# Kernel tuning notes

Measured on AMD Instinct MI355X. Metric: run time of the kernel, lower is better.

## Reference

```python
import jax, jax.numpy as jnp
import numpy as np

K = 3          # kernel_size (forced by hardcoded padding=1 in query unfold)
PAD = 1        # padding
C_IN = 64      # conv in_channels (x has C_IN + 5 channels)
C_OUT = 128    # out_channels
B, H, W = 16, 32, 32


def unfold(x, k, pad=0, mode='constant'):
    """torch.nn.functional.unfold equivalent. x: (B,C,H,W) -> (B, C*k*k, L).
    Ordering matches torch: channel slowest, then kernel row, then kernel col."""
    if pad:
        x = jnp.pad(x, ((0, 0), (0, 0), (pad, pad), (pad, pad)), mode=mode)
    b, c, h, w = x.shape
    oh, ow = h - k + 1, w - k + 1
    # (B, C, k*k, oh, ow) with patch index i*k+j
    patches = jnp.stack([x[:, :, i:i + oh, j:j + ow]
                         for i in range(k) for j in range(k)], axis=2)
    return patches.reshape(b, c * k * k, oh * ow)


def conv2d(x, w, b, pad):
    out = jax.lax.conv_general_dilated(
        x, w, window_strides=(1, 1), padding=[(pad, pad), (pad, pad)],
        dimension_numbers=('NCHW', 'OIHW', 'NCHW'))
    return out + b[None, :, None, None]


def setup_inputs() -> dict:
    key = jax.random.key(0)
    ks = jax.random.split(key, 6)
    fan1 = C_IN * K * K
    fan2 = C_OUT * 1 * 1
    return {
        'x': jax.random.normal(ks[0], (B, C_IN + 5, H, W), jnp.float32),
        'conv_w': jax.random.normal(ks[1], (C_OUT, C_IN, K, K), jnp.float32) / np.sqrt(fan1),
        'conv_b': jax.random.normal(ks[2], (C_OUT,), jnp.float32) * 0.01,
        'conv2_w': jax.random.normal(ks[3], (1, C_OUT, 1, 1), jnp.float32) / np.sqrt(fan2),
        'conv2_b': jax.random.normal(ks[4], (1,), jnp.float32) * 0.01,
        'shapes_kernel': jax.random.uniform(ks[5], (1, C_OUT, K * K * 5, 1), jnp.float32),
    }


def reference(x, conv_w, conv_b, conv2_w, conv2_b, shapes_kernel):
    k, pad = K, PAD
    center = k * k // 2

    conv_out = conv2d(x[:, :-5], conv_w, conv_b, pad)          # (B, C_OUT, H', W')
    b, cout, oh, ow = conv_out.shape
    L = oh * ow

    # shape-channel windows (replication-padded), center-relative positions
    sw = unfold(x[:, -5:], k, pad, 'edge').reshape(b, 5, k * k, L)
    sw = sw.at[:, 0:2].add(-sw[:, 0:2, center:center + 1])

    # L1 distance of each window to each learned shape kernel
    sd = jnp.abs(sw.reshape(b, 1, 5 * k * k, L) - shapes_kernel).sum(axis=2)  # (B, C_OUT, L)
    sd = sd.reshape(b, cout, oh, ow)

    saf = jax.nn.relu(conv_out / (sd + 1.0))                    # shape_attended_features

    q = conv2d(saf, conv2_w, conv2_b, 0) / jnp.sqrt(jnp.float32(cout))  # (B, 1, H', W')
    qu = jax.nn.softmax(unfold(q, k, 1), axis=1)[:, None]       # (B, 1, k*k, L), zero-padded

    u_mean = unfold(x[:, -5:-3], k, pad, 'edge').reshape(b, 2, k * k, L)
    means = (u_mean * qu).sum(axis=2)                           # (B, 2, L)

    v1 = (unfold(x[:, -3:-1], k, pad, 'edge').reshape(b, 2, k * k, L) * qu).sum(axis=2)
    v2 = (((u_mean - means[:, :, None, :]) ** 2) * qu).sum(axis=2)
    var = v1 + v2                                               # (B, 2, L)

    c1 = (unfold(x[:, -1:], k, pad, 'edge').reshape(b, 1, k * k, L) * qu).sum(axis=2)
    c2 = ((u_mean[:, 0:1] - means[:, 0:1, None, :]) *
          (u_mean[:, 1:2] - means[:, 1:2, None, :]) * qu).sum(axis=2)
    covar = c1 + c2                                             # (B, 1, L)

    agg = jnp.concatenate([means, var, covar], axis=1).reshape(b, 5, oh, ow)
    return jnp.concatenate([saf, agg], axis=1)                  # (B, C_OUT+5, H', W')
```

## Files before the change

kernel.cpp:

```cpp
#include <hip/hip_runtime.h>
#include <math.h>

#define CI 64
#define CO 128
#define CX 69
#define LPIX 1024

typedef __attribute__((ext_vector_type(8))) short bf16x8;
typedef __attribute__((ext_vector_type(4))) float f32x4;

#define WMF_OFF  0
#define SKT_OFF  147456
#define QP_OFF   (147456 + 23040)

__device__ __forceinline__ unsigned short f2bf(float f) {
  unsigned u = __float_as_uint(f);
  unsigned r = (u + 0x7fffu + ((u >> 16) & 1u)) >> 16;
  return (unsigned short)r;
}

__launch_bounds__(256)
__global__ void prepW(const float* __restrict__ cwg,
                      const float* __restrict__ skg,
                      unsigned short* __restrict__ wmf,
                      float* __restrict__ skt) {
  int i = blockIdx.x * 256 + threadIdx.x;
  if (i < 9 * 128 * 64) {
    int tap = i >> 13;
    int rem = i & 8191;
    int co = rem >> 6, cis = rem & 63;
    int ci = cis ^ ((co & 7) << 3);
    wmf[i] = f2bf(cwg[co * 576 + ci * 9 + tap]);
  } else {
    int d = i - 9 * 128 * 64;
    if (d < 45 * 128) {
      int j = d >> 7, co = d & 127;
      skt[j * 128 + co] = skg[co * 45 + j];
    }
  }
}

__launch_bounds__(256, 3)
__global__ void convFused(const float* __restrict__ xg,
                          const unsigned short* __restrict__ wmf,
                          const float* __restrict__ cbg,
                          const float* __restrict__ w2g,
                          const float* __restrict__ sktg,
                          float* __restrict__ qp,
                          float* __restrict__ outg) {
  __shared__ char arena[16384];
  __shared__ unsigned short ldsB[4 * 36 * 64];
  __shared__ float lds_sx[5 * 144];
  __shared__ float qred[4][64];

  unsigned short* A0 = (unsigned short*)arena;
  float* lds_c = (float*)arena;

  const int tid = threadIdx.x;
  const int blk = blockIdx.x;
  const int coh = blk & 1;
  const int rp  = (blk >> 1) & 15;
  const int b   = blk >> 5;
  const int r0  = rp * 2;

  const int w    = tid >> 6;
  const int lane = tid & 63;
  const int rsel = w >> 1;
  const int cq   = w & 1;
  const int n16  = lane & 15;
  const int kq   = lane >> 4;

  const float* xb = xg + (size_t)b * CX * LPIX;
  const float* xs = xb + CI * LPIX;

  {
    const int col = tid & 31;
    const int grp = tid >> 5;
    const int slot = col + 1;
    const int swk = (slot & 7) << 3;
    #pragma unroll
    for (int it = 0; it < 16; ++it) {
      const int rc  = grp + it * 8;
      const int row = rc >> 5;
      const int ci  = (rc & 31) * 2;
      const int grow = r0 - 1 + row;
      unsigned v = 0;
      if ((unsigned)grow < 32u) {
        float f0 = xb[ci * LPIX + grow * 32 + col];
        float f1 = xb[(ci + 1) * LPIX + grow * 32 + col];
        v = (unsigned)f2bf(f0) | ((unsigned)f2bf(f1) << 16);
      }
      const int gslot = ((ci >> 3) << 3) ^ swk;
      ((unsigned*)ldsB)[(((row * 36 + slot) << 6) + gslot + (ci & 7)) >> 1] = v;
    }
    for (int idx = tid; idx < 512; idx += 256) {
      const int row = idx >> 7;
      const int s4  = (idx >> 5) & 3;
      const int sl  = (s4 == 0) ? 0 : (32 + s4);
      const int ci  = (idx & 31) * 2;
      const int gsl = ((ci >> 3) << 3) ^ ((sl & 7) << 3);
      ((unsigned*)ldsB)[(((row * 36 + sl) << 6) + gsl + (ci & 7)) >> 1] = 0;
    }
  }

  for (int idx = tid; idx < 5 * 144; idx += 256) {
    int c = idx / 144, rem = idx - c * 144;
    int s = rem / 36, j = rem - s * 36;
    int hh = r0 - 1 + s; hh = hh < 0 ? 0 : (hh > 31 ? 31 : hh);
    int col = j - 1;     col = col < 0 ? 0 : (col > 31 ? 31 : col);
    lds_sx[idx] = xs[c * LPIX + hh * 32 + col];
  }

  {
    const uint4* s = (const uint4*)(wmf + (size_t)(coh * 64) * 64);
    uint4 v0 = s[tid], v1 = s[tid + 256];
    uint4* d = (uint4*)A0;
    d[tid] = v0; d[tid + 256] = v1;
  }
  __syncthreads();

  f32x4 acc[2][2] = {};

  for (int tap = 0; tap < 9; ++tap) {
    const int dr = tap / 3, dc = tap % 3;
    uint4 pf0, pf1;
    if (tap < 8) {
      const uint4* s = (const uint4*)(wmf + (size_t)((tap + 1) * 128 + coh * 64) * 64);
      pf0 = s[tid]; pf1 = s[tid + 256];
    }
    const int rowst = rsel + dr;
    const unsigned short* abase = A0 + (tap & 1) * 4096;
    #pragma unroll
    for (int ci0 = 0; ci0 < 64; ci0 += 32) {
      const int g = (ci0 >> 3) + kq;
      bf16x8 bfr[2];
      #pragma unroll
      for (int t = 0; t < 2; ++t) {
        const int slot = t * 16 + n16 + dc;
        const int gs = (g ^ (slot & 7)) << 3;
        bfr[t] = *(const bf16x8*)(ldsB + ((rowst * 36 + slot) << 6) + gs);
      }
      const int gsa = ((kq | (ci0 >> 3)) ^ (n16 & 7)) << 3;
      #pragma unroll
      for (int ct = 0; ct < 2; ++ct) {
        const int co_l = cq * 32 + ct * 16 + n16;
        bf16x8 a = *(const bf16x8*)(abase + co_l * 64 + gsa);
        acc[0][ct] = __builtin_amdgcn_mfma_f32_16x16x32_bf16(a, bfr[0], acc[0][ct], 0, 0, 0);
        acc[1][ct] = __builtin_amdgcn_mfma_f32_16x16x32_bf16(a, bfr[1], acc[1][ct], 0, 0, 0);
      }
    }
    if (tap < 8) {
      uint4* d = (uint4*)(A0 + ((tap + 1) & 1) * 4096);
      d[tid] = pf0; d[tid + 256] = pf1;
    }
    __syncthreads();
  }

  #pragma unroll
  for (int pt = 0; pt < 2; ++pt) {
    const int pxl = rsel * 32 + pt * 16 + n16;
    #pragma unroll
    for (int ct = 0; ct < 2; ++ct) {
      const int cog = cq * 8 + ct * 4 + kq;
      const int sg  = cog ^ (pxl & 7);
      *(f32x4*)&lds_c[pxl * 64 + sg * 4] = acc[pt][ct];
    }
  }
  __syncthreads();

  const int wS   = __builtin_amdgcn_readfirstlane(w);
  const int co0g = coh * 64 + wS * 16;
  const int pxl  = lane;

  float cvals[16];
  #pragma unroll
  for (int g = 0; g < 4; ++g) {
    const int cog = wS * 4 + g;
    const int sg  = cog ^ (pxl & 7);
    *(f32x4*)&cvals[g * 4] = *(const f32x4*)&lds_c[pxl * 64 + sg * 4];
  }

  const int xbase = (pxl >> 5) * 36 + (pxl & 31);
  float swv[45];
  {
    const float c0 = lds_sx[0 * 144 + 37 + xbase];
    const float c1 = lds_sx[1 * 144 + 37 + xbase];
    #pragma unroll
    for (int c = 0; c < 5; ++c) {
      float ctr = (c == 0) ? c0 : ((c == 1) ? c1 : 0.f);
      #pragma unroll
      for (int s = 0; s < 3; ++s)
        #pragma unroll
        for (int dc = 0; dc < 3; ++dc)
          swv[c * 9 + s * 3 + dc] = lds_sx[c * 144 + s * 36 + dc + xbase] - ctr;
    }
  }

  float sd[16];
  #pragma unroll
  for (int k = 0; k < 16; ++k) sd[k] = 0.f;
  const float* skt = sktg + co0g;
  #pragma unroll
  for (int j = 0; j < 45; ++j) {
    const float sv = swv[j];
    #pragma unroll
    for (int k = 0; k < 16; ++k)
      sd[k] += fabsf(sv - skt[j * 128 + k]);
  }

  float qpv = 0.f;
  float* ob = outg + ((size_t)b * 133 + co0g) * LPIX + (r0 + (pxl >> 5)) * 32 + (pxl & 31);
  #pragma unroll
  for (int k = 0; k < 16; ++k) {
    float v = (cvals[k] + cbg[co0g + k]) * __builtin_amdgcn_rcpf(sd[k] + 1.0f);
    v = v > 0.f ? v : 0.f;
    ob[(size_t)k * LPIX] = v;
    qpv = fmaf(v, w2g[co0g + k], qpv);
  }

  qred[w][lane] = qpv;
  __syncthreads();
  if (tid < 64) {
    float q = qred[0][tid] + qred[1][tid] + qred[2][tid] + qred[3][tid];
    qp[coh * 16384 + b * LPIX + r0 * 32 + tid] = q;
  }
}

__launch_bounds__(64)
__global__ void statsB(const float* __restrict__ xg,
                       const float* __restrict__ qp,
                       const float* __restrict__ b2g,
                       float* __restrict__ outg) {
  const int gid = blockIdx.x * 64 + threadIdx.x;
  const int b = gid >> 10;
  const int h = (gid >> 5) & 31;
  const int w = gid & 31;

  const float b2 = b2g[0];
  const float* q0 = qp + (size_t)b * LPIX;
  float qv[9];
  float m = -1e30f;
  #pragma unroll
  for (int t = 0; t < 9; ++t) {
    int hh = h + t / 3 - 1, wc = w + t % 3 - 1;
    float v = 0.f;
    if ((unsigned)hh < 32u && (unsigned)wc < 32u) {
      int off = hh * 32 + wc;
      v = (q0[off] + q0[16384 + off] + b2) * 0.08838834764831845f;
    }
    qv[t] = v;
    m = fmaxf(m, v);
  }
  float ssum = 0.f;
  #pragma unroll
  for (int t = 0; t < 9; ++t) { qv[t] = expf(qv[t] - m); ssum += qv[t]; }
  const float inv = 1.f / ssum;

  const float* xs = xg + ((size_t)b * CX + CI) * LPIX;
  float um0[9], um1[9];
  float m0 = 0.f, m1 = 0.f, v1a = 0.f, v1b = 0.f, c1 = 0.f;
  #pragma unroll
  for (int t = 0; t < 9; ++t) {
    int hh = h + t / 3 - 1; hh = hh < 0 ? 0 : (hh > 31 ? 31 : hh);
    int wc = w + t % 3 - 1; wc = wc < 0 ? 0 : (wc > 31 ? 31 : wc);
    int off = hh * 32 + wc;
    float quv = qv[t] * inv;
    qv[t] = quv;
    float a0 = xs[off];
    float a1 = xs[LPIX + off];
    float b0 = xs[2 * LPIX + off];
    float b1 = xs[3 * LPIX + off];
    float cc = xs[4 * LPIX + off];
    um0[t] = a0; um1[t] = a1;
    m0 = fmaf(a0, quv, m0);
    m1 = fmaf(a1, quv, m1);
    v1a = fmaf(b0, quv, v1a);
    v1b = fmaf(b1, quv, v1b);
    c1 = fmaf(cc, quv, c1);
  }
  float var0 = v1a, var1 = v1b, cov = c1;
  #pragma unroll
  for (int t = 0; t < 9; ++t) {
    float d0 = um0[t] - m0, d1 = um1[t] - m1;
    var0 = fmaf(d0 * d0, qv[t], var0);
    var1 = fmaf(d1 * d1, qv[t], var1);
    cov  = fmaf(d0 * d1, qv[t], cov);
  }
  float* ob = outg + ((size_t)b * 133 + 128) * LPIX + h * 32 + w;
  ob[0 * LPIX] = m0;
  ob[1 * LPIX] = m1;
  ob[2 * LPIX] = var0;
  ob[3 * LPIX] = var1;
  ob[4 * LPIX] = cov;
}

extern "C" void kernel_launch(void* const* d_in, const int* in_sizes, int n_in,
                              void* d_out, int out_size, void* d_ws, size_t ws_size,
                              hipStream_t stream) {
  const float* x  = (const float*)d_in[0];
  const float* cw = (const float*)d_in[1];
  const float* cb = (const float*)d_in[2];
  const float* w2 = (const float*)d_in[3];
  const float* b2 = (const float*)d_in[4];
  const float* sk = (const float*)d_in[5];
  float* out = (float*)d_out;

  unsigned short* wmf = (unsigned short*)((char*)d_ws + WMF_OFF);
  float* skt = (float*)((char*)d_ws + SKT_OFF);
  float* qp  = (float*)((char*)d_ws + QP_OFF);

  prepW<<<dim3(311), dim3(256), 0, stream>>>(cw, sk, wmf, skt);
  convFused<<<dim3(512), dim3(256), 0, stream>>>(x, wmf, cb, w2, skt, qp, out);
  statsB<<<dim3(256), dim3(64), 0, stream>>>(x, qp, b2, out);
}
```

Measured before the change: 32.18 us.

## Fuse softmax stats kernel into conv via atomic neighbor-completion counters

Removes the separate statsB launch. Each convFused block atomically increments per-(batch,row-pair) counters for its neighbor rows, and the last contributor computes the windowed softmax statistics for that row pair in-kernel. Counters are zeroed in prepW. This trades a kernel launch and its tail for atomics, threadfences and a serial tail inside some conv blocks. It relies on xs being defined in the hidden part of convFused.

```diff
diff --git a/kernel.cpp b/kernel.cpp
--- a/kernel.cpp
+++ b/kernel.cpp
@@ -12,6 +12,7 @@
 #define WMF_OFF  0
 #define SKT_OFF  147456
 #define QP_OFF   (147456 + 23040)
+#define CNT_OFF  (QP_OFF + 131072)
 
 __device__ __forceinline__ unsigned short f2bf(float f) {
   unsigned u = __float_as_uint(f);
@@ -23,7 +24,8 @@
 __global__ void prepW(const float* __restrict__ cwg,
                       const float* __restrict__ skg,
                       unsigned short* __restrict__ wmf,
-                      float* __restrict__ skt) {
+                      float* __restrict__ skt,
+                      int* __restrict__ cnt) {
   int i = blockIdx.x * 256 + threadIdx.x;
   if (i < 9 * 128 * 64) {
     int tap = i >> 13;
@@ -36,6 +38,9 @@
     if (d < 45 * 128) {
       int j = d >> 7, co = d & 127;
       skt[j * 128 + co] = skg[co * 45 + j];
+    } else {
+      int c = d - 45 * 128;
+      if (c < 256) cnt[c] = 0;
     }
   }
 }
@@ -45,13 +50,16 @@
                           const unsigned short* __restrict__ wmf,
                           const float* __restrict__ cbg,
                           const float* __restrict__ w2g,
+                          const float* __restrict__ b2g,
                           const float* __restrict__ sktg,
                           float* __restrict__ qp,
+                          int* __restrict__ cnt,
                           float* __restrict__ outg) {
   __shared__ char arena[16384];
   __shared__ unsigned short ldsB[4 * 36 * 64];
   __shared__ float lds_sx[5 * 144];
   __shared__ float qred[4][64];
+  __shared__ int jobs[3];
 
   unsigned short* A0 = (unsigned short*)arena;
   float* lds_c = (float*)arena;
@@ -224,74 +232,85 @@
     float q = qred[0][tid] + qred[1][tid] + qred[2][tid] + qred[3][tid];
     qp[coh * 16384 + b * LPIX + r0 * 32 + tid] = q;
   }
-}
-
-__launch_bounds__(64)
-__global__ void statsB(const float* __restrict__ xg,
-                       const float* __restrict__ qp,
-                       const float* __restrict__ b2g,
-                       float* __restrict__ outg) {
-  const int gid = blockIdx.x * 64 + threadIdx.x;
-  const int b = gid >> 10;
-  const int h = (gid >> 5) & 31;
-  const int w = gid & 31;
-
-  const float b2 = b2g[0];
-  const float* q0 = qp + (size_t)b * LPIX;
-  float qv[9];
-  float m = -1e30f;
-  #pragma unroll
-  for (int t = 0; t < 9; ++t) {
-    int hh = h + t / 3 - 1, wc = w + t % 3 - 1;
-    float v = 0.f;
-    if ((unsigned)hh < 32u && (unsigned)wc < 32u) {
-      int off = hh * 32 + wc;
-      v = (q0[off] + q0[16384 + off] + b2) * 0.08838834764831845f;
-    }
-    qv[t] = v;
-    m = fmaxf(m, v);
-  }
-  float ssum = 0.f;
-  #pragma unroll
-  for (int t = 0; t < 9; ++t) { qv[t] = expf(qv[t] - m); ssum += qv[t]; }
-  const float inv = 1.f / ssum;
-
-  const float* xs = xg + ((size_t)b * CX + CI) * LPIX;
-  float um0[9], um1[9];
-  float m0 = 0.f, m1 = 0.f, v1a = 0.f, v1b = 0.f, c1 = 0.f;
-  #pragma unroll
-  for (int t = 0; t < 9; ++t) {
-    int hh = h + t / 3 - 1; hh = hh < 0 ? 0 : (hh > 31 ? 31 : hh);
-    int wc = w + t % 3 - 1; wc = wc < 0 ? 0 : (wc > 31 ? 31 : wc);
-    int off = hh * 32 + wc;
-    float quv = qv[t] * inv;
-    qv[t] = quv;
-    float a0 = xs[off];
-    float a1 = xs[LPIX + off];
-    float b0 = xs[2 * LPIX + off];
-    float b1 = xs[3 * LPIX + off];
-    float cc = xs[4 * LPIX + off];
-    um0[t] = a0; um1[t] = a1;
-    m0 = fmaf(a0, quv, m0);
-    m1 = fmaf(a1, quv, m1);
-    v1a = fmaf(b0, quv, v1a);
-    v1b = fmaf(b1, quv, v1b);
-    c1 = fmaf(cc, quv, c1);
-  }
-  float var0 = v1a, var1 = v1b, cov = c1;
-  #pragma unroll
-  for (int t = 0; t < 9; ++t) {
-    float d0 = um0[t] - m0, d1 = um1[t] - m1;
-    var0 = fmaf(d0 * d0, qv[t], var0);
-    var1 = fmaf(d1 * d1, qv[t], var1);
-    cov  = fmaf(d0 * d1, qv[t], cov);
-  }
-  float* ob = outg + ((size_t)b * 133 + 128) * LPIX + h * 32 + w;
-  ob[0 * LPIX] = m0;
-  ob[1 * LPIX] = m1;
-  ob[2 * LPIX] = var0;
-  ob[3 * LPIX] = var1;
-  ob[4 * LPIX] = cov;
+  __syncthreads();
+
+  if (tid == 0) {
+    __threadfence();
+    jobs[0] = jobs[1] = jobs[2] = -1;
+    int n = 0;
+    const int lo = (rp == 0) ? 0 : rp - 1;
+    const int hi = (rp == 15) ? 15 : rp + 1;
+    for (int r = lo; r <= hi; ++r) {
+      const int tgt = (r == 0 || r == 15) ? 4 : 6;
+      int old = atomicAdd(&cnt[b * 16 + r], 1);
+      if (old == tgt - 1) jobs[n++] = r;
+    }
+    __threadfence();
+  }
+  __syncthreads();
+
+  const int job = (w < 3) ? jobs[w] : -1;
+  if (job >= 0) {
+    const int h   = job * 2 + (lane >> 5);
+    const int wcx = lane & 31;
+    const float b2 = b2g[0];
+    const float* qb0 = qp + (size_t)b * LPIX;
+    const float* qb1 = qb0 + 16384;
+
+    float qv[9];
+    float mm = -1e30f;
+    #pragma unroll
+    for (int t = 0; t < 9; ++t) {
+      int hh = h + t / 3 - 1, wc2 = wcx + t % 3 - 1;
+      float v = 0.f;
+      if ((unsigned)hh < 32u && (unsigned)wc2 < 32u) {
+        int off = hh * 32 + wc2;
+        v = (qb0[off] + qb1[off] + b2) * 0.08838834764831845f;
+      }
+      qv[t] = v;
+      mm = fmaxf(mm, v);
+    }
+    float ssum = 0.f;
+    #pragma unroll
+    for (int t = 0; t < 9; ++t) { qv[t] = expf(qv[t] - mm); ssum += qv[t]; }
+    const float inv = 1.f / ssum;
+
+    float um0[9], um1[9];
+    float m0 = 0.f, m1 = 0.f, v1a = 0.f, v1b = 0.f, c1 = 0.f;
+    #pragma unroll
+    for (int t = 0; t < 9; ++t) {
+      int hh = h + t / 3 - 1; hh = hh < 0 ? 0 : (hh > 31 ? 31 : hh);
+      int wc2 = wcx + t % 3 - 1; wc2 = wc2 < 0 ? 0 : (wc2 > 31 ? 31 : wc2);
+      int off = hh * 32 + wc2;
+      float quv = qv[t] * inv;
+      qv[t] = quv;
+      float a0 = xs[off];
+      float a1 = xs[LPIX + off];
+      float b0 = xs[2 * LPIX + off];
+      float b1 = xs[3 * LPIX + off];
+      float cc = xs[4 * LPIX + off];
+      um0[t] = a0; um1[t] = a1;
+      m0 = fmaf(a0, quv, m0);
+      m1 = fmaf(a1, quv, m1);
+      v1a = fmaf(b0, quv, v1a);
+      v1b = fmaf(b1, quv, v1b);
+      c1 = fmaf(cc, quv, c1);
+    }
+    float var0 = v1a, var1 = v1b, cov = c1;
+    #pragma unroll
+    for (int t = 0; t < 9; ++t) {
+      float d0 = um0[t] - m0, d1 = um1[t] - m1;
+      var0 = fmaf(d0 * d0, qv[t], var0);
+      var1 = fmaf(d1 * d1, qv[t], var1);
+      cov  = fmaf(d0 * d1, qv[t], cov);
+    }
+    float* ob2 = outg + ((size_t)b * 133 + 128) * LPIX + h * 32 + wcx;
+    ob2[0 * LPIX] = m0;
+    ob2[1 * LPIX] = m1;
+    ob2[2 * LPIX] = var0;
+    ob2[3 * LPIX] = var1;
+    ob2[4 * LPIX] = cov;
+  }
 }
 
 extern "C" void kernel_launch(void* const* d_in, const int* in_sizes, int n_in,
@@ -308,8 +327,8 @@
   unsigned short* wmf = (unsigned short*)((char*)d_ws + WMF_OFF);
   float* skt = (float*)((char*)d_ws + SKT_OFF);
   float* qp  = (float*)((char*)d_ws + QP_OFF);
-
-  prepW<<<dim3(311), dim3(256), 0, stream>>>(cw, sk, wmf, skt);
-  convFused<<<dim3(512), dim3(256), 0, stream>>>(x, wmf, cb, w2, skt, qp, out);
-  statsB<<<dim3(256), dim3(64), 0, stream>>>(x, qp, b2, out);
+  int*   cnt = (int*)((char*)d_ws + CNT_OFF);
+
+  prepW<<<dim3(312), dim3(256), 0, stream>>>(cw, sk, wmf, skt, cnt);
+  convFused<<<dim3(512), dim3(256), 0, stream>>>(x, wmf, cb, w2, b2, skt, qp, cnt, out);
 }
```

Result: slower. 50.40 us (+56.6%).

## Load conv weights directly from global memory into MFMA operands, dropping LDS staging

Applied to the files above, without the earlier changes.

The weight matrix is re-laid out as co-major with taps and channels contiguous, so each lane can read its bf16x8 A fragment straight from global/L2 instead of staging per-tap weight tiles through double-buffered LDS. This removes the per-tap barrier and LDS stores from the tap loop, which is now fully unrolled. The B tile shares one arena with the output staging buffer. The trade-off is more global/L2 load traffic and latency per MFMA, plus higher register use, with the occupancy hint lowered from 3 to 2 blocks per CU.

```diff
diff --git a/kernel.cpp b/kernel.cpp
--- a/kernel.cpp
+++ b/kernel.cpp
@@ -25,14 +25,12 @@
                       unsigned short* __restrict__ wmf,
                       float* __restrict__ skt) {
   int i = blockIdx.x * 256 + threadIdx.x;
-  if (i < 9 * 128 * 64) {
-    int tap = i >> 13;
-    int rem = i & 8191;
-    int co = rem >> 6, cis = rem & 63;
-    int ci = cis ^ ((co & 7) << 3);
+  if (i < 128 * 9 * 64) {
+    int co = i / 576, rem = i - co * 576;
+    int tap = rem >> 6, ci = rem & 63;
     wmf[i] = f2bf(cwg[co * 576 + ci * 9 + tap]);
   } else {
-    int d = i - 9 * 128 * 64;
+    int d = i - 128 * 9 * 64;
     if (d < 45 * 128) {
       int j = d >> 7, co = d & 127;
       skt[j * 128 + co] = skg[co * 45 + j];
@@ -40,20 +38,19 @@
   }
 }
 
-__launch_bounds__(256, 3)
+__launch_bounds__(256, 2)
 __global__ void convFused(const float* __restrict__ xg,
-                          const unsigned short* __restrict__ wmf,
+                          const unsigned short* __restrict__ wmfg,
                           const float* __restrict__ cbg,
                           const float* __restrict__ w2g,
                           const float* __restrict__ sktg,
                           float* __restrict__ qp,
                           float* __restrict__ outg) {
-  __shared__ char arena[16384];
-  __shared__ unsigned short ldsB[4 * 36 * 64];
+  __shared__ char arena[18432];
   __shared__ float lds_sx[5 * 144];
   __shared__ float qred[4][64];
 
-  unsigned short* A0 = (unsigned short*)arena;
+  unsigned short* ldsB = (unsigned short*)arena;
   float* lds_c = (float*)arena;
 
   const int tid = threadIdx.x;
@@ -110,29 +107,25 @@
     int col = j - 1;     col = col < 0 ? 0 : (col > 31 ? 31 : col);
     lds_sx[idx] = xs[c * LPIX + hh * 32 + col];
   }
-
-  {
-    const uint4* s = (const uint4*)(wmf + (size_t)(coh * 64) * 64);
-    uint4 v0 = s[tid], v1 = s[tid + 256];
-    uint4* d = (uint4*)A0;
-    d[tid] = v0; d[tid + 256] = v1;
-  }
   __syncthreads();
 
+  const unsigned short* ap[2][2];
+  #pragma unroll
+  for (int ch = 0; ch < 2; ++ch)
+    #pragma unroll
+    for (int ct = 0; ct < 2; ++ct)
+      ap[ch][ct] = wmfg + (size_t)(coh * 64 + cq * 32 + ct * 16 + n16) * 576
+                   + ch * 32 + kq * 8;
+
   f32x4 acc[2][2] = {};
 
+  #pragma unroll
   for (int tap = 0; tap < 9; ++tap) {
     const int dr = tap / 3, dc = tap % 3;
-    uint4 pf0, pf1;
-    if (tap < 8) {
-      const uint4* s = (const uint4*)(wmf + (size_t)((tap + 1) * 128 + coh * 64) * 64);
-      pf0 = s[tid]; pf1 = s[tid + 256];
-    }
     const int rowst = rsel + dr;
-    const unsigned short* abase = A0 + (tap & 1) * 4096;
-    #pragma unroll
-    for (int ci0 = 0; ci0 < 64; ci0 += 32) {
-      const int g = (ci0 >> 3) + kq;
+    #pragma unroll
+    for (int ch = 0; ch < 2; ++ch) {
+      const int g = (ch << 2) + kq;
       bf16x8 bfr[2];
       #pragma unroll
       for (int t = 0; t < 2; ++t) {
@@ -140,21 +133,15 @@
         const int gs = (g ^ (slot & 7)) << 3;
         bfr[t] = *(const bf16x8*)(ldsB + ((rowst * 36 + slot) << 6) + gs);
       }
-      const int gsa = ((kq | (ci0 >> 3)) ^ (n16 & 7)) << 3;
       #pragma unroll
       for (int ct = 0; ct < 2; ++ct) {
-        const int co_l = cq * 32 + ct * 16 + n16;
-        bf16x8 a = *(const bf16x8*)(abase + co_l * 64 + gsa);
+        bf16x8 a = *(const bf16x8*)(ap[ch][ct] + tap * 64);
         acc[0][ct] = __builtin_amdgcn_mfma_f32_16x16x32_bf16(a, bfr[0], acc[0][ct], 0, 0, 0);
         acc[1][ct] = __builtin_amdgcn_mfma_f32_16x16x32_bf16(a, bfr[1], acc[1][ct], 0, 0, 0);
       }
     }
-    if (tap < 8) {
-      uint4* d = (uint4*)(A0 + ((tap + 1) & 1) * 4096);
-      d[tid] = pf0; d[tid + 256] = pf1;
-    }
-    __syncthreads();
-  }
+  }
+  __syncthreads();
 
   #pragma unroll
   for (int pt = 0; pt < 2; ++pt) {
```

New measurement: 36.95 us. +14.8%, slower.
